# Performance work log

Measured on AMD Instinct MI355X. Metric: run time of the kernel, lower is better.

The kernel has to match this reference:

```python
import jax, jax.numpy as jnp
import numpy as np

N = 10000          # nodes
E = 320000         # edges (avg degree 32)
D_IN = 64          # node_pos feature width
NS, NG, NV = 128, 128, 128   # gate: scalars, gates, gated channels
NTYPES = 8         # edge types
FC = 64            # fc_neurons hidden width
D_OUT = 64
NUM_NEIGHBORS = 32.0


def setup_inputs() -> dict:
    key = jax.random.key(0)
    ks = jax.random.split(key, 32)
    inp = {}
    inp["node_pos"] = jax.random.normal(ks[0], (N, D_IN), dtype=jnp.float32)
    dims_in = [D_IN, D_IN + NS + NV, D_IN + NS + NV]     # 64, 320, 320
    dims_out = [NS + NG + NV, NS + NG + NV, D_OUT]       # 384, 384, 64
    i = 1
    for l in range(3):
        di, do = dims_in[l], dims_out[l]
        inp[f"w_self_{l}"] = jax.random.normal(ks[i], (di, do), dtype=jnp.float32) / np.sqrt(di); i += 1
        inp[f"w_msg_{l}"] = jax.random.normal(ks[i], (di, do), dtype=jnp.float32) / np.sqrt(di); i += 1
        inp[f"fc0_{l}"] = jax.random.normal(ks[i], (NTYPES, FC), dtype=jnp.float32) / np.sqrt(NTYPES); i += 1
        inp[f"fc1_{l}"] = jax.random.normal(ks[i], (FC, FC), dtype=jnp.float32) / np.sqrt(FC); i += 1
        inp[f"fc2_{l}"] = jax.random.normal(ks[i], (FC, do), dtype=jnp.float32) / np.sqrt(FC); i += 1
    inp["edge_src"] = jax.random.randint(ks[i], (E,), 0, N); i += 1
    inp["edge_dst"] = jax.random.randint(ks[i], (E,), 0, N); i += 1
    inp["edge_type"] = jax.random.randint(ks[i], (E,), 0, NTYPES)
    return inp


def _conv(x, edge_src, edge_dst, etype_onehot, w_self, w_msg, f0, f1, f2):
    # fc_neurons MLP on edge attrs -> per-edge tensor-product weights [E, out]
    w = jax.nn.silu(etype_onehot @ f0)
    w = jax.nn.silu(w @ f1)
    w = w @ f2
    # gather source node features, weighted message, scatter-sum to dst
    msg = (x[edge_src] @ w_msg) * w                       # [E, out]
    agg = jax.ops.segment_sum(msg, edge_dst, num_segments=N)
    agg = agg / jnp.sqrt(jnp.asarray(NUM_NEIGHBORS, x.dtype))
    return x @ w_self + agg                               # self-connection + messages


def _gate(h):
    # e3nn Gate: scalars -> silu, gates -> sigmoid, gated channels modulated by gates
    s = h[:, :NS]
    g = h[:, NS:NS + NG]
    v = h[:, NS + NG:]
    return jnp.concatenate([jax.nn.silu(s), v * jax.nn.sigmoid(g)], axis=-1)


def reference(node_pos,
              w_self_0, w_msg_0, fc0_0, fc1_0, fc2_0,
              w_self_1, w_msg_1, fc0_1, fc1_1, fc2_1,
              w_self_2, w_msg_2, fc0_2, fc1_2, fc2_2,
              edge_src, edge_dst, edge_type):
    etype_onehot = jax.nn.one_hot(edge_type, NTYPES, dtype=node_pos.dtype)
    mid = node_pos
    params = [(w_self_0, w_msg_0, fc0_0, fc1_0, fc2_0),
              (w_self_1, w_msg_1, fc0_1, fc1_1, fc2_1)]
    for w_self, w_msg, f0, f1, f2 in params:
        h = _conv(mid, edge_src, edge_dst, etype_onehot, w_self, w_msg, f0, f1, f2)
        mid = jnp.concatenate([node_pos, _gate(h)], axis=-1)   # concated_tensor
    return _conv(mid, edge_src, edge_dst, etype_onehot, w_self_2, w_msg_2, fc0_2, fc1_2, fc2_2)
```

## Files before the change

kernel.cpp:

```cpp
#include <hip/hip_runtime.h>
#include <hip/hip_bf16.h>

#define N_NODES 10000
#define N_EDGES 320000
#define NTYPES 8
#define FC 64
#define SLOTS 96

using short8v = __attribute__((ext_vector_type(8))) short;
using f32x4   = __attribute__((ext_vector_type(4))) float;

__device__ __forceinline__ float sigmoidf_(float x) { return 1.f / (1.f + expf(-x)); }

__device__ __forceinline__ unsigned short f2bf(float x) {
    union { float f; unsigned u; } un; un.f = x;
    unsigned r = un.u + 0x7fff + ((un.u >> 16) & 1);
    return (unsigned short)(r >> 16);
}
__device__ __forceinline__ float bf2f(unsigned short b) {
    union { unsigned u; float f; } un; un.u = ((unsigned)b) << 16;
    return un.f;
}
__device__ __forceinline__ float bflo(unsigned d) {
    union { unsigned u; float f; } un; un.u = d << 16; return un.f;
}
__device__ __forceinline__ float bfhi(unsigned d) {
    union { unsigned u; float f; } un; un.u = d & 0xffff0000u; return un.f;
}
__device__ __forceinline__ unsigned packbf(float lo, float hi) {
    return (unsigned)f2bf(lo) | ((unsigned)f2bf(hi) << 16);
}

__device__ __forceinline__ void wtrans(const float* __restrict__ in,
                                       unsigned short* __restrict__ out,
                                       int K, int Nn, int idx) {
    int n = idx / K, k = idx - n * K;
    out[idx] = f2bf(in[k * Nn + n]);
}

__global__ void prep_misc(const float* __restrict__ node_pos,
                          const float* __restrict__ w0, const float* __restrict__ w1,
                          const float* __restrict__ w2, const float* __restrict__ w3,
                          const float* __restrict__ w4, const float* __restrict__ w5,
                          int* __restrict__ cnt, unsigned short* __restrict__ np16,
                          unsigned short* __restrict__ o0, unsigned short* __restrict__ o1,
                          unsigned short* __restrict__ o2, unsigned short* __restrict__ o3,
                          unsigned short* __restrict__ o4, unsigned short* __restrict__ o5) {
    int idx = blockIdx.x * 256 + threadIdx.x;
    if (idx < N_NODES) { cnt[idx] = 0; return; }
    idx -= N_NODES;
    if (idx < N_NODES * 64) { np16[idx] = f2bf(node_pos[idx]); return; }
    idx -= N_NODES * 64;
    if (idx < 24576) { wtrans(w0, o0, 64, 384, idx); return; }
    idx -= 24576;
    if (idx < 24576) { wtrans(w1, o1, 64, 384, idx); return; }
    idx -= 24576;
    if (idx < 122880) { wtrans(w2, o2, 320, 384, idx); return; }
    idx -= 122880;
    if (idx < 122880) { wtrans(w3, o3, 320, 384, idx); return; }
    idx -= 122880;
    if (idx < 20480) { wtrans(w4, o4, 320, 64, idx); return; }
    idx -= 20480;
    if (idx < 20480) { wtrans(w5, o5, 320, 64, idx); return; }
}
#define PREP_TOTAL (N_NODES + N_NODES * 64 + 2 * 24576 + 2 * 122880 + 2 * 20480)

__global__ void fill_kernel(const int* __restrict__ esrc, const int* __restrict__ edst,
                            const int* __restrict__ etype, int* __restrict__ cnt,
                            int* __restrict__ csr) {
    int e = blockIdx.x * 256 + threadIdx.x;
    if (e >= N_EDGES) return;
    int d = edst[e];
    int pos = atomicAdd(&cnt[d], 1);
    if (pos < SLOTS) csr[d * SLOTS + pos] = esrc[e] * 8 + etype[e];
}

__global__ void wtab_fused(const float* __restrict__ f0_0, const float* __restrict__ f1_0,
                           const float* __restrict__ f2_0,
                           const float* __restrict__ f0_1, const float* __restrict__ f1_1,
                           const float* __restrict__ f2_1,
                           const float* __restrict__ f0_2, const float* __restrict__ f1_2,
                           const float* __restrict__ f2_2,
                           float* __restrict__ wtab0, float* __restrict__ wtab1,
                           float* __restrict__ wtab2) {
    const int tid = threadIdx.x;
    const int bb = blockIdx.x;
    const float *f0, *f1, *f2;
    float* wtab;
    int dout, idx;
    if (bb < 12)      { f0 = f0_0; f1 = f1_0; f2 = f2_0; wtab = wtab0; dout = 384; idx = bb * 256 + tid; }
    else if (bb < 24) { f0 = f0_1; f1 = f1_1; f2 = f2_1; wtab = wtab1; dout = 384; idx = (bb - 12) * 256 + tid; }
    else              { f0 = f0_2; f1 = f1_2; f2 = f2_2; wtab = wtab2; dout = 64;  idx = (bb - 24) * 256 + tid; }
    __shared__ float a[NTYPES * FC];
    __shared__ float bs[NTYPES * FC];
    for (int i = tid; i < NTYPES * FC; i += 256) { float v = f0[i]; a[i] = v * sigmoidf_(v); }
    __syncthreads();
    for (int i = tid; i < NTYPES * FC; i += 256) {
        int t = i >> 6, j = i & 63;
        float s = 0.f;
        #pragma unroll
        for (int k = 0; k < FC; ++k) s = fmaf(a[t * FC + k], f1[k * FC + j], s);
        bs[i] = s * sigmoidf_(s);
    }
    __syncthreads();
    if (idx >= NTYPES * dout) return;
    int t = idx / dout, c = idx - t * dout;
    float s = 0.f;
    #pragma unroll
    for (int k = 0; k < FC; ++k) s = fmaf(bs[t * FC + k], f2[k * dout + c], s);
    wtab[idx] = s * 0.17677669529663687f;
}

__global__ __launch_bounds__(256) void mfma_dual(
        const unsigned short* __restrict__ A,
        const unsigned short* __restrict__ BtS, const unsigned short* __restrict__ BtM,
        float* __restrict__ Cs, unsigned short* __restrict__ Cm,
        int M, int K, int N, int nct) {
    int by = blockIdx.y;
    const bool is_msg = (by >= nct);
    const unsigned short* Bt = is_msg ? BtM : BtS;
    if (is_msg) by -= nct;
    const int wave = threadIdx.x >> 6;
    const int lane = threadIdx.x & 63;
    const int r16 = lane & 15;
    const int kg  = lane >> 4;
    const int rowBase = blockIdx.x * 128 + wave * 32;
    const int colBase = by * 64;

    f32x4 acc[2][4] = {};
    for (int k0 = 0; k0 < K; k0 += 32) {
        short8v a[2], b[4];
        #pragma unroll
        for (int mi = 0; mi < 2; ++mi) {
            int r = rowBase + mi * 16 + r16;
            if (r >= M) r = M - 1;
            a[mi] = *reinterpret_cast<const short8v*>(&A[(long long)r * K + k0 + kg * 8]);
        }
        #pragma unroll
        for (int nj = 0; nj < 4; ++nj) {
            int c = colBase + nj * 16 + r16;
            b[nj] = *reinterpret_cast<const short8v*>(&Bt[(long long)c * K + k0 + kg * 8]);
        }
        #pragma unroll
        for (int mi = 0; mi < 2; ++mi)
            #pragma unroll
            for (int nj = 0; nj < 4; ++nj)
                acc[mi][nj] = __builtin_amdgcn_mfma_f32_16x16x32_bf16(
                                  a[mi], b[nj], acc[mi][nj], 0, 0, 0);
    }
    #pragma unroll
    for (int mi = 0; mi < 2; ++mi) {
        #pragma unroll
        for (int j = 0; j < 4; ++j) {
            int r = rowBase + mi * 16 + kg * 4 + j;
            if (r >= M) continue;
            #pragma unroll
            for (int nj = 0; nj < 4; ++nj) {
                int c = colBase + nj * 16 + r16;
                float v = acc[mi][nj][j];
                if (is_msg) Cm[(long long)r * N + c] = f2bf(v);
                else        Cs[(long long)r * N + c] = v;
            }
        }
    }
}

__global__ void gather_gate(const unsigned short* __restrict__ ymsg,
                            const float* __restrict__ yself,
                            const unsigned short* __restrict__ np16,
                            const float* __restrict__ wtab,
                            const int* __restrict__ cnt,
                            const int* __restrict__ csr,
                            unsigned short* __restrict__ mid16) {
    __shared__ float wt[NTYPES * 384];
    const int tid = threadIdx.x;
    for (int i = tid; i < NTYPES * 384; i += 256) wt[i] = wtab[i];
    __syncthreads();
    const int node = blockIdx.x * 4 + (tid >> 6);
    const int lane = tid & 63;
    if (node >= N_NODES) return;
    int deg = cnt[node];
    if (deg > SLOTS) deg = SLOTS;
    const int* __restrict__ row = csr + node * SLOTS;
    const unsigned* __restrict__ y32 = (const unsigned*)ymsg;
    const float2* __restrict__ wt2 = (const float2*)wt;
    float acc[3][2] = {};
    int i = 0;
    for (; i + 3 < deg; i += 4) {
        int p0 = row[i], p1 = row[i + 1], p2 = row[i + 2], p3 = row[i + 3];
        unsigned b0 = (unsigned)(p0 >> 3) * 192u + lane, t0 = (unsigned)(p0 & 7) * 192u + lane;
        unsigned b1 = (unsigned)(p1 >> 3) * 192u + lane, t1 = (unsigned)(p1 & 7) * 192u + lane;
        unsigned b2 = (unsigned)(p2 >> 3) * 192u + lane, t2 = (unsigned)(p2 & 7) * 192u + lane;
        unsigned b3 = (unsigned)(p3 >> 3) * 192u + lane, t3 = (unsigned)(p3 & 7) * 192u + lane;
        #pragma unroll
        for (int j = 0; j < 3; ++j) {
            const unsigned o = j * 64;
            unsigned d0 = y32[b0 + o]; float2 w0 = wt2[t0 + o];
            unsigned d1 = y32[b1 + o]; float2 w1 = wt2[t1 + o];
            unsigned d2 = y32[b2 + o]; float2 w2 = wt2[t2 + o];
            unsigned d3 = y32[b3 + o]; float2 w3 = wt2[t3 + o];
            acc[j][0] = fmaf(bflo(d0), w0.x, acc[j][0]);
            acc[j][1] = fmaf(bfhi(d0), w0.y, acc[j][1]);
            acc[j][0] = fmaf(bflo(d1), w1.x, acc[j][0]);
            acc[j][1] = fmaf(bfhi(d1), w1.y, acc[j][1]);
            acc[j][0] = fmaf(bflo(d2), w2.x, acc[j][0]);
            acc[j][1] = fmaf(bfhi(d2), w2.y, acc[j][1]);
            acc[j][0] = fmaf(bflo(d3), w3.x, acc[j][0]);
            acc[j][1] = fmaf(bfhi(d3), w3.y, acc[j][1]);
        }
    }
    for (; i < deg; ++i) {
        int p0 = row[i];
        unsigned b0 = (unsigned)(p0 >> 3) * 192u + lane, t0 = (unsigned)(p0 & 7) * 192u + lane;
        #pragma unroll
        for (int j = 0; j < 3; ++j) {
            unsigned d0 = y32[b0 + j * 64]; float2 w0 = wt2[t0 + j * 64];
            acc[j][0] = fmaf(bflo(d0), w0.x, acc[j][0]);
            acc[j][1] = fmaf(bfhi(d0), w0.y, acc[j][1]);
        }
    }
    const float2* __restrict__ ysv = (const float2*)(yself + (long long)node * 384);
    float h[3][2];
    #pragma unroll
    for (int j = 0; j < 3; ++j) {
        float2 ys = ysv[j * 64 + lane];
        h[j][0] = ys.x + acc[j][0];
        h[j][1] = ys.y + acc[j][1];
    }
    unsigned* __restrict__ m32 = (unsigned*)(mid16 + (long long)node * 320);
    const unsigned* __restrict__ np32 = (const unsigned*)np16;
    if (lane < 32) m32[lane] = np32[node * 32 + lane];
    m32[32 + lane] = packbf(h[0][0] * sigmoidf_(h[0][0]),
                            h[0][1] * sigmoidf_(h[0][1]));
    m32[96 + lane] = packbf(h[2][0] * sigmoidf_(h[1][0]),
                            h[2][1] * sigmoidf_(h[1][1]));
}

__global__ void gather_final(const unsigned short* __restrict__ ymsg,
                             const float* __restrict__ yself,
                             const float* __restrict__ wtab,
                             const int* __restrict__ cnt,
                             const int* __restrict__ csr,
                             float* __restrict__ out) {
    __shared__ float wt[NTYPES * 64];
    const int tid = threadIdx.x;
    for (int i = tid; i < NTYPES * 64; i += 256) wt[i] = wtab[i];
    __syncthreads();
    const int node = blockIdx.x * 4 + (tid >> 6);
    const int lane = tid & 63;
    if (node >= N_NODES) return;
    int deg = cnt[node];
    if (deg > SLOTS) deg = SLOTS;
    const int* __restrict__ row = csr + node * SLOTS;
    const unsigned* __restrict__ y32 = (const unsigned*)ymsg;
    const float2* __restrict__ wt2 = (const float2*)wt;
    const int half = lane >> 5, cl = lane & 31;
    float a0 = 0.f, a1 = 0.f;
    int i = 0;
    for (; i + 7 < deg; i += 8) {
        #pragma unroll
        for (int q = 0; q < 4; ++q) {
            int p = row[i + 2 * q + half];
            unsigned d = y32[(unsigned)(p >> 3) * 32u + cl];
            float2 w = wt2[(unsigned)(p & 7) * 32u + cl];
            a0 = fmaf(bflo(d), w.x, a0);
            a1 = fmaf(bfhi(d), w.y, a1);
        }
    }
    for (; i + 1 < deg; i += 2) {
        int p = row[i + half];
        unsigned d = y32[(unsigned)(p >> 3) * 32u + cl];
        float2 w = wt2[(unsigned)(p & 7) * 32u + cl];
        a0 = fmaf(bflo(d), w.x, a0);
        a1 = fmaf(bfhi(d), w.y, a1);
    }
    if (i < deg) {
        if (half == 0) {
            int p = row[i];
            unsigned d = y32[(unsigned)(p >> 3) * 32u + cl];
            float2 w = wt2[(unsigned)(p & 7) * 32u + cl];
            a0 = fmaf(bflo(d), w.x, a0);
            a1 = fmaf(bfhi(d), w.y, a1);
        }
    }
    a0 += __shfl_xor(a0, 32);
    a1 += __shfl_xor(a1, 32);
    if (half == 0) {
        float2 o;
        o.x = yself[(long long)node * 64 + 2 * cl]     + a0;
        o.y = yself[(long long)node * 64 + 2 * cl + 1] + a1;
        reinterpret_cast<float2*>(out)[(long long)node * 32 + cl] = o;
    }
}

extern "C" void kernel_launch(void* const* d_in, const int* in_sizes, int n_in,
                              void* d_out, int out_size, void* d_ws, size_t ws_size,
                              hipStream_t stream) {
    const float* node_pos = (const float*)d_in[0];
    const float* w_self[3] = {(const float*)d_in[1], (const float*)d_in[6],  (const float*)d_in[11]};
    const float* w_msg[3]  = {(const float*)d_in[2], (const float*)d_in[7],  (const float*)d_in[12]};
    const float* fc0[3]    = {(const float*)d_in[3], (const float*)d_in[8],  (const float*)d_in[13]};
    const float* fc1[3]    = {(const float*)d_in[4], (const float*)d_in[9],  (const float*)d_in[14]};
    const float* fc2[3]    = {(const float*)d_in[5], (const float*)d_in[10], (const float*)d_in[15]};
    const int* esrc  = (const int*)d_in[16];
    const int* edst  = (const int*)d_in[17];
    const int* etype = (const int*)d_in[18];
    float* out = (float*)d_out;

    float* f = (float*)d_ws;
    float* wtab0 = f; f += NTYPES * 384;
    float* wtab1 = f; f += NTYPES * 384;
    float* wtab2 = f; f += NTYPES * 64;
    float* yself = f; f += (long long)N_NODES * 384;
    unsigned short* u = (unsigned short*)f;
    unsigned short* ymsg16 = u; u += (long long)N_NODES * 384;
    unsigned short* mid16  = u; u += (long long)N_NODES * 320;
    unsigned short* np16   = u; u += (long long)N_NODES * 64;
    unsigned short* bt0s = u; u += 64 * 384;
    unsigned short* bt0m = u; u += 64 * 384;
    unsigned short* bt1s = u; u += 320 * 384;
    unsigned short* bt1m = u; u += 320 * 384;
    unsigned short* bt2s = u; u += 320 * 64;
    unsigned short* bt2m = u; u += 320 * 64;
    int* ip = (int*)u;
    int* cnt = ip; ip += N_NODES;
    int* csr = ip; ip += (long long)N_NODES * SLOTS;

    prep_misc<<<(PREP_TOTAL + 255) / 256, 256, 0, stream>>>(
        node_pos, w_self[0], w_msg[0], w_self[1], w_msg[1], w_self[2], w_msg[2],
        cnt, np16, bt0s, bt0m, bt1s, bt1m, bt2s, bt2m);

    fill_kernel<<<(N_EDGES + 255) / 256, 256, 0, stream>>>(esrc, edst, etype, cnt, csr);

    wtab_fused<<<26, 256, 0, stream>>>(fc0[0], fc1[0], fc2[0],
                                       fc0[1], fc1[1], fc2[1],
                                       fc0[2], fc1[2], fc2[2],
                                       wtab0, wtab1, wtab2);

    const int ggrid_n = (N_NODES + 3) / 4;
    const int mrows = (N_NODES + 127) / 128;

    {
        dim3 g(mrows, 2 * (384 / 64));
        mfma_dual<<<g, 256, 0, stream>>>(np16, bt0s, bt0m, yself, ymsg16,
                                         N_NODES, 64, 384, 384 / 64);
        gather_gate<<<ggrid_n, 256, 0, stream>>>(ymsg16, yself, np16, wtab0, cnt, csr, mid16);
    }
    {
        dim3 g(mrows, 2 * (384 / 64));
        mfma_dual<<<g, 256, 0, stream>>>(mid16, bt1s, bt1m, yself, ymsg16,
                                         N_NODES, 320, 384, 384 / 64);
        gather_gate<<<ggrid_n, 256, 0, stream>>>(ymsg16, yself, np16, wtab1, cnt, csr, mid16);
    }
    {
        dim3 g(mrows, 2 * (64 / 64));
        mfma_dual<<<g, 256, 0, stream>>>(mid16, bt2s, bt2m, yself, ymsg16,
                                         N_NODES, 320, 64, 64 / 64);
        gather_final<<<ggrid_n, 256, 0, stream>>>(ymsg16, yself, wtab2, cnt, csr, out);
    }
}
```

Measured before the change: 180.1 us.

## Merge prep kernels, vectorize CSR fill, split gather edges across two waves

The weight-table MLP kernel is folded into the prep kernel, which saves one launch. The CSR fill kernel now handles four edges per thread using int4 loads. gather_gate now runs two waves per node, each summing half the edge list, and combines the partial sums through shared memory. This raises parallelism on the latency-bound gather, at the cost of an extra block barrier and shared-memory traffic; the int4 row loads rely on 16-byte alignment of the split point.

New measurement: 171.2 us. 1.05x faster.

```diff
diff --git a/kernel.cpp b/kernel.cpp
--- a/kernel.cpp
+++ b/kernel.cpp
@@ -17,10 +17,6 @@
     unsigned r = un.u + 0x7fff + ((un.u >> 16) & 1);
     return (unsigned short)(r >> 16);
 }
-__device__ __forceinline__ float bf2f(unsigned short b) {
-    union { unsigned u; float f; } un; un.u = ((unsigned)b) << 16;
-    return un.f;
-}
 __device__ __forceinline__ float bflo(unsigned d) {
     union { unsigned u; float f; } un; un.u = d << 16; return un.f;
 }
@@ -38,15 +34,54 @@
     out[idx] = f2bf(in[k * Nn + n]);
 }
 
-__global__ void prep_misc(const float* __restrict__ node_pos,
-                          const float* __restrict__ w0, const float* __restrict__ w1,
-                          const float* __restrict__ w2, const float* __restrict__ w3,
-                          const float* __restrict__ w4, const float* __restrict__ w5,
-                          int* __restrict__ cnt, unsigned short* __restrict__ np16,
-                          unsigned short* __restrict__ o0, unsigned short* __restrict__ o1,
-                          unsigned short* __restrict__ o2, unsigned short* __restrict__ o3,
-                          unsigned short* __restrict__ o4, unsigned short* __restrict__ o5) {
-    int idx = blockIdx.x * 256 + threadIdx.x;
+#define PREP_TOTAL (N_NODES + N_NODES * 64 + 2 * 24576 + 2 * 122880 + 2 * 20480)
+
+__global__ void prep_all(const float* __restrict__ node_pos,
+                         const float* __restrict__ w0, const float* __restrict__ w1,
+                         const float* __restrict__ w2, const float* __restrict__ w3,
+                         const float* __restrict__ w4, const float* __restrict__ w5,
+                         const float* __restrict__ f0_0, const float* __restrict__ f1_0,
+                         const float* __restrict__ f2_0,
+                         const float* __restrict__ f0_1, const float* __restrict__ f1_1,
+                         const float* __restrict__ f2_1,
+                         const float* __restrict__ f0_2, const float* __restrict__ f1_2,
+                         const float* __restrict__ f2_2,
+                         int* __restrict__ cnt, unsigned short* __restrict__ np16,
+                         unsigned short* __restrict__ o0, unsigned short* __restrict__ o1,
+                         unsigned short* __restrict__ o2, unsigned short* __restrict__ o3,
+                         unsigned short* __restrict__ o4, unsigned short* __restrict__ o5,
+                         float* __restrict__ wtab0, float* __restrict__ wtab1,
+                         float* __restrict__ wtab2) {
+    const int tid = threadIdx.x;
+    const int bb = blockIdx.x;
+    if (bb < 26) {
+        const float *f0, *f1, *f2;
+        float* wtab;
+        int dout, idx;
+        if (bb < 12)      { f0 = f0_0; f1 = f1_0; f2 = f2_0; wtab = wtab0; dout = 384; idx = bb * 256 + tid; }
+        else if (bb < 24) { f0 = f0_1; f1 = f1_1; f2 = f2_1; wtab = wtab1; dout = 384; idx = (bb - 12) * 256 + tid; }
+        else              { f0 = f0_2; f1 = f1_2; f2 = f2_2; wtab = wtab2; dout = 64;  idx = (bb - 24) * 256 + tid; }
+        __shared__ float a[NTYPES * FC];
+        __shared__ float bs[NTYPES * FC];
+        for (int i = tid; i < NTYPES * FC; i += 256) { float v = f0[i]; a[i] = v * sigmoidf_(v); }
+        __syncthreads();
+        for (int i = tid; i < NTYPES * FC; i += 256) {
+            int t = i >> 6, j = i & 63;
+            float s = 0.f;
+            #pragma unroll
+            for (int k = 0; k < FC; ++k) s = fmaf(a[t * FC + k], f1[k * FC + j], s);
+            bs[i] = s * sigmoidf_(s);
+        }
+        __syncthreads();
+        if (idx >= NTYPES * dout) return;
+        int t = idx / dout, c = idx - t * dout;
+        float s = 0.f;
+        #pragma unroll
+        for (int k = 0; k < FC; ++k) s = fmaf(bs[t * FC + k], f2[k * dout + c], s);
+        wtab[idx] = s * 0.17677669529663687f;
+        return;
+    }
+    int idx = (bb - 26) * 256 + tid;
     if (idx < N_NODES) { cnt[idx] = 0; return; }
     idx -= N_NODES;
     if (idx < N_NODES * 64) { np16[idx] = f2bf(node_pos[idx]); return; }
@@ -63,52 +98,20 @@
     idx -= 20480;
     if (idx < 20480) { wtrans(w5, o5, 320, 64, idx); return; }
 }
-#define PREP_TOTAL (N_NODES + N_NODES * 64 + 2 * 24576 + 2 * 122880 + 2 * 20480)
 
 __global__ void fill_kernel(const int* __restrict__ esrc, const int* __restrict__ edst,
                             const int* __restrict__ etype, int* __restrict__ cnt,
                             int* __restrict__ csr) {
-    int e = blockIdx.x * 256 + threadIdx.x;
-    if (e >= N_EDGES) return;
-    int d = edst[e];
-    int pos = atomicAdd(&cnt[d], 1);
-    if (pos < SLOTS) csr[d * SLOTS + pos] = esrc[e] * 8 + etype[e];
-}
-
-__global__ void wtab_fused(const float* __restrict__ f0_0, const float* __restrict__ f1_0,
-                           const float* __restrict__ f2_0,
-                           const float* __restrict__ f0_1, const float* __restrict__ f1_1,
-                           const float* __restrict__ f2_1,
-                           const float* __restrict__ f0_2, const float* __restrict__ f1_2,
-                           const float* __restrict__ f2_2,
-                           float* __restrict__ wtab0, float* __restrict__ wtab1,
-                           float* __restrict__ wtab2) {
-    const int tid = threadIdx.x;
-    const int bb = blockIdx.x;
-    const float *f0, *f1, *f2;
-    float* wtab;
-    int dout, idx;
-    if (bb < 12)      { f0 = f0_0; f1 = f1_0; f2 = f2_0; wtab = wtab0; dout = 384; idx = bb * 256 + tid; }
-    else if (bb < 24) { f0 = f0_1; f1 = f1_1; f2 = f2_1; wtab = wtab1; dout = 384; idx = (bb - 12) * 256 + tid; }
-    else              { f0 = f0_2; f1 = f1_2; f2 = f2_2; wtab = wtab2; dout = 64;  idx = (bb - 24) * 256 + tid; }
-    __shared__ float a[NTYPES * FC];
-    __shared__ float bs[NTYPES * FC];
-    for (int i = tid; i < NTYPES * FC; i += 256) { float v = f0[i]; a[i] = v * sigmoidf_(v); }
-    __syncthreads();
-    for (int i = tid; i < NTYPES * FC; i += 256) {
-        int t = i >> 6, j = i & 63;
-        float s = 0.f;
-        #pragma unroll
-        for (int k = 0; k < FC; ++k) s = fmaf(a[t * FC + k], f1[k * FC + j], s);
-        bs[i] = s * sigmoidf_(s);
-    }
-    __syncthreads();
-    if (idx >= NTYPES * dout) return;
-    int t = idx / dout, c = idx - t * dout;
-    float s = 0.f;
-    #pragma unroll
-    for (int k = 0; k < FC; ++k) s = fmaf(bs[t * FC + k], f2[k * dout + c], s);
-    wtab[idx] = s * 0.17677669529663687f;
+    int e4 = (blockIdx.x * 256 + threadIdx.x) * 4;
+    if (e4 >= N_EDGES) return;
+    int4 s = *reinterpret_cast<const int4*>(&esrc[e4]);
+    int4 d = *reinterpret_cast<const int4*>(&edst[e4]);
+    int4 t = *reinterpret_cast<const int4*>(&etype[e4]);
+    int p;
+    p = atomicAdd(&cnt[d.x], 1); if (p < SLOTS) csr[d.x * SLOTS + p] = s.x * 8 + t.x;
+    p = atomicAdd(&cnt[d.y], 1); if (p < SLOTS) csr[d.y * SLOTS + p] = s.y * 8 + t.y;
+    p = atomicAdd(&cnt[d.z], 1); if (p < SLOTS) csr[d.z * SLOTS + p] = s.z * 8 + t.z;
+    p = atomicAdd(&cnt[d.w], 1); if (p < SLOTS) csr[d.w * SLOTS + p] = s.w * 8 + t.w;
 }
 
 __global__ __launch_bounds__(256) void mfma_dual(
@@ -165,33 +168,42 @@
     }
 }
 
-__global__ void gather_gate(const unsigned short* __restrict__ ymsg,
-                            const float* __restrict__ yself,
-                            const unsigned short* __restrict__ np16,
-                            const float* __restrict__ wtab,
-                            const int* __restrict__ cnt,
-                            const int* __restrict__ csr,
-                            unsigned short* __restrict__ mid16) {
+__global__ __launch_bounds__(512) void gather_gate(
+        const unsigned short* __restrict__ ymsg,
+        const float* __restrict__ yself,
+        const unsigned short* __restrict__ np16,
+        const float* __restrict__ wtab,
+        const int* __restrict__ cnt,
+        const int* __restrict__ csr,
+        unsigned short* __restrict__ mid16) {
     __shared__ float wt[NTYPES * 384];
+    __shared__ float sacc[4][6][64];
     const int tid = threadIdx.x;
-    for (int i = tid; i < NTYPES * 384; i += 256) wt[i] = wtab[i];
-    __syncthreads();
-    const int node = blockIdx.x * 4 + (tid >> 6);
+    for (int i = tid; i < NTYPES * 384; i += 512) wt[i] = wtab[i];
+    const int wv = tid >> 6;
     const int lane = tid & 63;
-    if (node >= N_NODES) return;
+    const int nib = wv >> 1;
+    const int sub = wv & 1;
+    const int node = blockIdx.x * 4 + nib;
     int deg = cnt[node];
     if (deg > SLOTS) deg = SLOTS;
+    int h = (((deg + 1) >> 1) + 3) & ~3;
+    if (h > deg) h = deg;
+    const int e0 = sub ? h : 0;
+    const int e1 = sub ? deg : h;
     const int* __restrict__ row = csr + node * SLOTS;
     const unsigned* __restrict__ y32 = (const unsigned*)ymsg;
     const float2* __restrict__ wt2 = (const float2*)wt;
+    __syncthreads();
+
     float acc[3][2] = {};
-    int i = 0;
-    for (; i + 3 < deg; i += 4) {
-        int p0 = row[i], p1 = row[i + 1], p2 = row[i + 2], p3 = row[i + 3];
-        unsigned b0 = (unsigned)(p0 >> 3) * 192u + lane, t0 = (unsigned)(p0 & 7) * 192u + lane;
-        unsigned b1 = (unsigned)(p1 >> 3) * 192u + lane, t1 = (unsigned)(p1 & 7) * 192u + lane;
-        unsigned b2 = (unsigned)(p2 >> 3) * 192u + lane, t2 = (unsigned)(p2 & 7) * 192u + lane;
-        unsigned b3 = (unsigned)(p3 >> 3) * 192u + lane, t3 = (unsigned)(p3 & 7) * 192u + lane;
+    int i = e0;
+    for (; i + 3 < e1; i += 4) {
+        int4 p = *reinterpret_cast<const int4*>(&row[i]);
+        unsigned b0 = (unsigned)(p.x >> 3) * 192u + lane, t0 = (unsigned)(p.x & 7) * 192u + lane;
+        unsigned b1 = (unsigned)(p.y >> 3) * 192u + lane, t1 = (unsigned)(p.y & 7) * 192u + lane;
+        unsigned b2 = (unsigned)(p.z >> 3) * 192u + lane, t2 = (unsigned)(p.z & 7) * 192u + lane;
+        unsigned b3 = (unsigned)(p.w >> 3) * 192u + lane, t3 = (unsigned)(p.w & 7) * 192u + lane;
         #pragma unroll
         for (int j = 0; j < 3; ++j) {
             const unsigned o = j * 64;
@@ -209,7 +221,7 @@
             acc[j][1] = fmaf(bfhi(d3), w3.y, acc[j][1]);
         }
     }
-    for (; i < deg; ++i) {
+    for (; i < e1; ++i) {
         int p0 = row[i];
         unsigned b0 = (unsigned)(p0 >> 3) * 192u + lane, t0 = (unsigned)(p0 & 7) * 192u + lane;
         #pragma unroll
@@ -219,21 +231,30 @@
             acc[j][1] = fmaf(bfhi(d0), w0.y, acc[j][1]);
         }
     }
+    if (sub == 1) {
+        #pragma unroll
+        for (int j = 0; j < 3; ++j) {
+            sacc[nib][2 * j][lane]     = acc[j][0];
+            sacc[nib][2 * j + 1][lane] = acc[j][1];
+        }
+    }
+    __syncthreads();
+    if (sub == 1) return;
     const float2* __restrict__ ysv = (const float2*)(yself + (long long)node * 384);
-    float h[3][2];
+    float h2[3][2];
     #pragma unroll
     for (int j = 0; j < 3; ++j) {
         float2 ys = ysv[j * 64 + lane];
-        h[j][0] = ys.x + acc[j][0];
-        h[j][1] = ys.y + acc[j][1];
+        h2[j][0] = ys.x + acc[j][0] + sacc[nib][2 * j][lane];
+        h2[j][1] = ys.y + acc[j][1] + sacc[nib][2 * j + 1][lane];
     }
     unsigned* __restrict__ m32 = (unsigned*)(mid16 + (long long)node * 320);
     const unsigned* __restrict__ np32 = (const unsigned*)np16;
     if (lane < 32) m32[lane] = np32[node * 32 + lane];
-    m32[32 + lane] = packbf(h[0][0] * sigmoidf_(h[0][0]),
-                            h[0][1] * sigmoidf_(h[0][1]));
-    m32[96 + lane] = packbf(h[2][0] * sigmoidf_(h[1][0]),
-                            h[2][1] * sigmoidf_(h[1][1]));
+    m32[32 + lane] = packbf(h2[0][0] * sigmoidf_(h2[0][0]),
+                            h2[0][1] * sigmoidf_(h2[0][1]));
+    m32[96 + lane] = packbf(h2[2][0] * sigmoidf_(h2[1][0]),
+                            h2[2][1] * sigmoidf_(h2[1][1]));
 }
 
 __global__ void gather_final(const unsigned short* __restrict__ ymsg,
@@ -326,36 +347,32 @@
     int* cnt = ip; ip += N_NODES;
     int* csr = ip; ip += (long long)N_NODES * SLOTS;
 
-    prep_misc<<<(PREP_TOTAL + 255) / 256, 256, 0, stream>>>(
+    prep_all<<<26 + (PREP_TOTAL + 255) / 256, 256, 0, stream>>>(
         node_pos, w_self[0], w_msg[0], w_self[1], w_msg[1], w_self[2], w_msg[2],
-        cnt, np16, bt0s, bt0m, bt1s, bt1m, bt2s, bt2m);
-
-    fill_kernel<<<(N_EDGES + 255) / 256, 256, 0, stream>>>(esrc, edst, etype, cnt, csr);
-
-    wtab_fused<<<26, 256, 0, stream>>>(fc0[0], fc1[0], fc2[0],
-                                       fc0[1], fc1[1], fc2[1],
-                                       fc0[2], fc1[2], fc2[2],
-                                       wtab0, wtab1, wtab2);
-
-    const int ggrid_n = (N_NODES + 3) / 4;
+        fc0[0], fc1[0], fc2[0], fc0[1], fc1[1], fc2[1], fc0[2], fc1[2], fc2[2],
+        cnt, np16, bt0s, bt0m, bt1s, bt1m, bt2s, bt2m, wtab0, wtab1, wtab2);
+
+    fill_kernel<<<(N_EDGES / 4 + 255) / 256, 256, 0, stream>>>(esrc, edst, etype, cnt, csr);
+
     const int mrows = (N_NODES + 127) / 128;
+    const int ggrid = N_NODES / 4;
 
     {
         dim3 g(mrows, 2 * (384 / 64));
         mfma_dual<<<g, 256, 0, stream>>>(np16, bt0s, bt0m, yself, ymsg16,
                                          N_NODES, 64, 384, 384 / 64);
-        gather_gate<<<ggrid_n, 256, 0, stream>>>(ymsg16, yself, np16, wtab0, cnt, csr, mid16);
+        gather_gate<<<ggrid, 512, 0, stream>>>(ymsg16, yself, np16, wtab0, cnt, csr, mid16);
     }
     {
         dim3 g(mrows, 2 * (384 / 64));
         mfma_dual<<<g, 256, 0, stream>>>(mid16, bt1s, bt1m, yself, ymsg16,
                                          N_NODES, 320, 384, 384 / 64);
-        gather_gate<<<ggrid_n, 256, 0, stream>>>(ymsg16, yself, np16, wtab1, cnt, csr, mid16);
+        gather_gate<<<ggrid, 512, 0, stream>>>(ymsg16, yself, np16, wtab1, cnt, csr, mid16);
     }
     {
         dim3 g(mrows, 2 * (64 / 64));
         mfma_dual<<<g, 256, 0, stream>>>(mid16, bt2s, bt2m, yself, ymsg16,
                                          N_NODES, 320, 64, 64 / 64);
-        gather_final<<<ggrid_n, 256, 0, stream>>>(ymsg16, yself, wtab2, cnt, csr, out);
-    }
-}
+        gather_final<<<(N_NODES + 3) / 4, 256, 0, stream>>>(ymsg16, yself, wtab2, cnt, csr, out);
+    }
+}
```
